# Kernel optimization log

Measured on AMD Instinct MI355X. Metric: run time of the kernel, lower is better.

The kernel has to match this reference:

```python
import jax, jax.numpy as jnp
import numpy as np

ALPHA = 0.5
INV_COEFF = 25.0
STD_COEFF = 25.0
COV_COEFF = 1.0
NUM_MATCHES = 50
EPS = 1e-5
GAMMA = 1.0


def _cdist(a, b):
    # (B,M,C),(B,N,C) -> (B,M,N) euclidean, matmul-based like torch.cdist
    a2 = jnp.sum(a * a, axis=-1, keepdims=True)            # (B,M,1)
    b2 = jnp.sum(b * b, axis=-1, keepdims=True)            # (B,N,1)
    d2 = a2 + jnp.swapaxes(b2, -1, -2) - 2.0 * jnp.einsum('bmc,bnc->bmn', a, b)
    return jnp.sqrt(jnp.maximum(d2, 0.0))


def _nn_match(input_maps, candidate_maps, distances, num_matches):
    # topk(k=1, largest=False) == min/argmin over last dim
    nn_dists = jnp.min(distances, axis=-1)                 # (B,M)
    nn_indices = jnp.argmin(distances, axis=-1)            # (B,M)
    # k smallest nn_dists, ascending order
    _, best_input_idx = jax.lax.top_k(-nn_dists, num_matches)   # (B,k)
    best_cand_idx = jnp.take_along_axis(nn_indices, best_input_idx, axis=1)
    filt_in = jnp.take_along_axis(input_maps, best_input_idx[:, :, None], axis=1)
    filt_cand = jnp.take_along_axis(candidate_maps, best_cand_idx[:, :, None], axis=1)
    return filt_in, filt_cand


def _off_diag_sq_sum(c):
    return jnp.sum(c * c) - jnp.sum(jnp.diag(c) ** 2)


def _std_term(x_flat):
    # unbiased variance over sample dim (torch var default)
    std = jnp.sqrt(jnp.var(x_flat, axis=0, ddof=1) + EPS)
    return jnp.mean(jax.nn.relu(GAMMA - std)) / 2.0


def _cov_term(x_flat):
    n, c = x_flat.shape
    xc = x_flat - jnp.mean(x_flat, axis=0)
    cov = xc.T @ xc / (n - 1)
    return _off_diag_sq_sum(cov) / c


def _vicreg_global(x, y):
    inv = jnp.mean((x - y) ** 2)
    std = _std_term(x) + _std_term(y)
    cov = _cov_term(x) + _cov_term(y)
    return INV_COEFF * inv + STD_COEFF * std + COV_COEFF * cov


def _vicregl_maps(x, y):
    # x, y: (B, k, C)
    inv = jnp.mean((x - y) ** 2)
    xf = x.reshape(-1, x.shape[-1])
    yf = y.reshape(-1, y.shape[-1])
    std = _std_term(xf) + _std_term(yf)
    cov = _cov_term(xf) + _cov_term(yf)
    return INV_COEFF * inv, STD_COEFF * std, COV_COEFF * cov


def _local_loss(spatial_1, spatial_2):
    B, C, H, W = spatial_1.shape
    maps_1 = spatial_1.reshape(B, C, H * W).transpose(0, 2, 1)   # (B,HW,C)
    maps_2 = spatial_2.reshape(B, C, H * W).transpose(0, 2, 1)
    d12 = _cdist(maps_1, maps_2)
    m1f, m1n = _nn_match(maps_1, maps_2, d12, NUM_MATCHES)
    d21 = _cdist(maps_2, maps_1)
    m2f, m2n = _nn_match(maps_2, maps_1, d21, NUM_MATCHES)
    inv1, var1, cov1 = _vicregl_maps(m1f, m1n)
    inv2, var2, cov2 = _vicregl_maps(m2f, m2n)
    return (inv1 + inv2) / 2 + (var1 + var2) / 2 + (cov1 + cov2) / 2


def setup_inputs() -> dict:
    key = jax.random.key(0)
    k1, k2, k3, k4 = jax.random.split(key, 4)
    B, C, H, W = 64, 768, 24, 24
    return {
        'spatial_1': jax.random.normal(k1, (B, C, H, W), dtype=jnp.float32),
        'pooled_1': jax.random.normal(k2, (B, C), dtype=jnp.float32),
        'spatial_2': jax.random.normal(k3, (B, C, H, W), dtype=jnp.float32),
        'pooled_2': jax.random.normal(k4, (B, C), dtype=jnp.float32),
    }


def reference(spatial_1, pooled_1, spatial_2, pooled_2):
    global_loss = _vicreg_global(pooled_1, pooled_2)
    local_loss = _local_loss(spatial_1, spatial_2)
    return ALPHA * global_loss + (1.0 - ALPHA) * local_loss
```

## Files before the change

kernel.cpp:

```cpp
#include <hip/hip_runtime.h>
#include <stdint.h>

typedef unsigned long long ull;
typedef unsigned int uint;
typedef unsigned short ushort;

typedef __attribute__((ext_vector_type(8))) short short8;
typedef __attribute__((ext_vector_type(4))) float floatx4;

#define B   64
#define C   768
#define HW  576
#define K   50
#define NLOC (B*K)

#define OFF_SLOTS   0
#define OFF_COLSUM  256
#define OFF_NN1     18688
#define OFF_NN2     313600
#define OFF_SELP    608512
#define OFF_SELQ    634112
#define OFF_NORM    659712
#define OFF_XT      954624
#define OFF_MP      OFF_XT
#define OFF_XGT     114200832
#define OFF_M       133861632

#define SLOT_INVG 0
#define SLOT_STD  1
#define SLOT_COV  7
#define SLOT_INV1 13
#define SLOT_INV2 14

__device__ __forceinline__ ull umin64(ull a, ull b) { return a < b ? a : b; }

__device__ __forceinline__ float bf2f_lo(uint u) { return __uint_as_float(u << 16); }
__device__ __forceinline__ float bf2f_hi(uint u) { return __uint_as_float(u & 0xffff0000u); }
__device__ __forceinline__ float bf2f(ushort u) { return __uint_as_float(((uint)u) << 16); }

__device__ __forceinline__ ushort f2bf(float f) {
    uint u = __float_as_uint(f);
    uint r = (u + 0x7fffu + ((u >> 16) & 1u)) >> 16;
    return (ushort)r;
}

__device__ __forceinline__ float blk_reduce_sum(float v, float* s4) {
    for (int off = 32; off > 0; off >>= 1) v += __shfl_down(v, off, 64);
    int lane = threadIdx.x & 63, w = threadIdx.x >> 6;
    if (lane == 0) s4[w] = v;
    __syncthreads();
    float r = 0.f;
    if (threadIdx.x == 0) r = s4[0] + s4[1] + s4[2] + s4[3];
    return r;
}

__global__ __launch_bounds__(256) void convert_kernel(const float* __restrict__ x1,
                                                      const float* __restrict__ x2,
                                                      ushort* __restrict__ xT,
                                                      float* __restrict__ norm) {
    int z = blockIdx.z;
    int which = z >> 6, b = z & 63;
    const float* X = which ? x2 : x1;
    int p0 = blockIdx.x * 64, c0 = blockIdx.y * 64;
    __shared__ float tile[64][65];
    const float* src = X + ((size_t)b * C + c0) * HW + p0;
    int col = threadIdx.x & 63, r0 = threadIdx.x >> 6;
    for (int rr = r0; rr < 64; rr += 4)
        tile[rr][col] = src[(size_t)rr * HW + col];
    __syncthreads();
    ushort* dst = xT + (((size_t)which * B + b) * HW + p0) * C + c0;
    int cc = (threadIdx.x & 31) * 2, pr0 = threadIdx.x >> 5;
    for (int pr = pr0; pr < 64; pr += 8) {
        ushort2 o;
        o.x = f2bf(tile[cc][pr]);
        o.y = f2bf(tile[cc + 1][pr]);
        *(ushort2*)&dst[(size_t)pr * C + cc] = o;
    }
    int p = threadIdx.x >> 2, g = threadIdx.x & 3;
    float s = 0.f;
    for (int c = g * 16; c < g * 16 + 16; ++c) {
        float v = bf2f(f2bf(tile[c][p]));
        s = fmaf(v, v, s);
    }
    s += __shfl_down(s, 2, 4);
    s += __shfl_down(s, 1, 4);
    if (g == 0) atomicAdd(&norm[((size_t)which * B + b) * HW + p0 + p], s);
}

__global__ __launch_bounds__(256) void cdist_mfma(const ushort* __restrict__ xT,
                                                  const float* __restrict__ norm,
                                                  ull* __restrict__ nn1,
                                                  ull* __restrict__ nn2) {
    int id = blockIdx.x;
    int xcd = id & 7, slot = id >> 3;
    int b = xcd + 8 * (slot / 25);
    int t = slot % 25;
    int qt = t % 5, pt = t / 5;

    const ushort* X1 = xT + (size_t)b * HW * C;
    const ushort* X2 = xT + (size_t)(B + b) * HW * C;

    __shared__ ull pool[4224];
    char* As = (char*)pool;
    char* Bs = As + 16384;

    int tid = threadIdx.x;
    int w = tid >> 6, l = tid & 63;
    int quad = l >> 4, col = l & 15;
    int lrow = l >> 2, pos = l & 3;

    const ushort* gA[2][2]; const ushort* gB[2][2];
    char* dA[2][2]; char* dB[2][2];
#pragma unroll
    for (int n = 0; n < 2; ++n) {
        int sm = w * 32 + n * 16 + lrow;
        int cdat = pos ^ ((sm >> 1) & 3);
        int p = pt * 128 + sm; if (p >= HW) p = HW - 1;
        int q = qt * 128 + sm; if (q >= HW) q = HW - 1;
#pragma unroll
        for (int s = 0; s < 2; ++s) {
            gA[s][n] = X1 + (size_t)p * C + s * 32 + cdat * 8;
            gB[s][n] = X2 + (size_t)q * C + s * 32 + cdat * 8;
            dA[s][n] = As + s * 8192 + w * 2048 + n * 1024;
            dB[s][n] = Bs + s * 8192 + w * 2048 + n * 1024;
        }
    }

    int offA[4], offB[4];
#pragma unroll
    for (int i = 0; i < 4; ++i) {
        int m_loc = (w >> 1) * 64 + i * 16 + col;
        offA[i] = m_loc * 64 + ((quad ^ ((m_loc >> 1) & 3)) * 16);
        int n_loc = (w & 1) * 64 + i * 16 + col;
        offB[i] = n_loc * 64 + ((quad ^ ((n_loc >> 1) & 3)) * 16);
    }

    floatx4 zero = {0.f, 0.f, 0.f, 0.f};
    floatx4 acc[4][4];
#pragma unroll
    for (int i = 0; i < 4; ++i)
#pragma unroll
        for (int j = 0; j < 4; ++j) acc[i][j] = zero;

    for (int k0 = 0; k0 < C; k0 += 64) {
        __syncthreads();
#pragma unroll
        for (int s = 0; s < 2; ++s)
#pragma unroll
            for (int n = 0; n < 2; ++n) {
                __builtin_amdgcn_global_load_lds(
                    (const __attribute__((address_space(1))) void*)(gA[s][n] + k0),
                    (__attribute__((address_space(3))) void*)dA[s][n], 16, 0, 0);
                __builtin_amdgcn_global_load_lds(
                    (const __attribute__((address_space(1))) void*)(gB[s][n] + k0),
                    (__attribute__((address_space(3))) void*)dB[s][n], 16, 0, 0);
            }
        __syncthreads();
#pragma unroll
        for (int s = 0; s < 2; ++s) {
            short8 a[4], bb[4];
#pragma unroll
            for (int i = 0; i < 4; ++i) a[i] = *(const short8*)(As + s * 8192 + offA[i]);
#pragma unroll
            for (int j = 0; j < 4; ++j) bb[j] = *(const short8*)(Bs + s * 8192 + offB[j]);
#pragma unroll
            for (int i = 0; i < 4; ++i)
#pragma unroll
                for (int j = 0; j < 4; ++j)
                    acc[i][j] = __builtin_amdgcn_mfma_f32_16x16x32_bf16(a[i], bb[j], acc[i][j], 0, 0, 0);
        }
    }

    const float* n1g = norm + (size_t)b * HW;
    const float* n2g = norm + (size_t)(B + b) * HW;
    float n1v[4][4]; bool vp[4][4];
    float n2v[4];    bool vq[4];
#pragma unroll
    for (int i = 0; i < 4; ++i)
#pragma unroll
        for (int r = 0; r < 4; ++r) {
            int p = pt * 128 + (w >> 1) * 64 + i * 16 + quad * 4 + r;
            vp[i][r] = (p < HW);
            n1v[i][r] = n1g[p < HW ? p : (HW - 1)];
        }
#pragma unroll
    for (int j = 0; j < 4; ++j) {
        int q = qt * 128 + (w & 1) * 64 + j * 16 + col;
        vq[j] = (q < HW);
        n2v[j] = n2g[q < HW ? q : (HW - 1)];
    }

    __syncthreads();
    typedef ull row33[33];
    row33* red = (row33*)pool;

#pragma unroll
    for (int i = 0; i < 4; ++i)
#pragma unroll
        for (int r = 0; r < 4; ++r) {
            int p_loc = (w >> 1) * 64 + i * 16 + quad * 4 + r;
            ull best = ~0ull;
#pragma unroll
            for (int j = 0; j < 4; ++j) {
                if (!vq[j]) continue;
                float d2 = fmaxf(n1v[i][r] + n2v[j] - 2.0f * acc[i][j][r], 0.0f);
                unsigned q_glob = qt * 128 + (w & 1) * 64 + j * 16 + col;
                best = umin64(best, ((ull)__float_as_uint(d2) << 32) | q_glob);
            }
            red[p_loc][(w & 1) * 16 + col] = best;
        }
    __syncthreads();
    if (tid < 128) {
        int p_glob = pt * 128 + tid;
        ull m = ~0ull;
#pragma unroll
        for (int x = 0; x < 32; ++x) m = umin64(m, red[tid][x]);
        if (p_glob < HW) atomicMin(&nn1[(size_t)b * HW + p_glob], m);
    }
    __syncthreads();
#pragma unroll
    for (int j = 0; j < 4; ++j) {
        int q_loc = (w & 1) * 64 + j * 16 + col;
        ull best = ~0ull;
#pragma unroll
        for (int i = 0; i < 4; ++i)
#pragma unroll
            for (int r = 0; r < 4; ++r) {
                if (!vp[i][r]) continue;
                float d2 = fmaxf(n1v[i][r] + n2v[j] - 2.0f * acc[i][j][r], 0.0f);
                unsigned p_glob = pt * 128 + (w >> 1) * 64 + i * 16 + quad * 4 + r;
                best = umin64(best, ((ull)__float_as_uint(d2) << 32) | p_glob);
            }
        red[q_loc][(w >> 1) * 4 + quad] = best;
    }
    __syncthreads();
    if (tid < 128) {
        int q_glob = qt * 128 + tid;
        ull m = ~0ull;
#pragma unroll
        for (int x = 0; x < 8; ++x) m = umin64(m, red[tid][x]);
        if (q_glob < HW) atomicMin(&nn2[(size_t)b * HW + q_glob], m);
    }
}

__global__ __launch_bounds__(64) void select_topk_wave(const ull* __restrict__ nn1,
                                                       const ull* __restrict__ nn2,
                                                       int* __restrict__ sel_p,
                                                       int* __restrict__ sel_q) {
    int b = blockIdx.x, dir = blockIdx.y;
    const ull* nn = dir ? nn2 : nn1;
    int lane = threadIdx.x;
    ull key[9]; uint qv[9];
#pragma unroll
    for (int r = 0; r < 9; ++r) {
        int p = r * 64 + lane;
        ull e = nn[(size_t)b * HW + p];
        key[r] = (e & 0xFFFFFFFF00000000ull) | (unsigned)p;
        qv[r] = (uint)(e & 0xFFFFFFFFu);
    }
    int* sp = sel_p + (dir * B + b) * K;
    int* sq = sel_q + (dir * B + b) * K;
    for (int it = 0; it < K; ++it) {
        ull m = key[0];
#pragma unroll
        for (int r = 1; r < 9; ++r) m = umin64(m, key[r]);
#pragma unroll
        for (int off = 32; off > 0; off >>= 1) m = umin64(m, __shfl_xor(m, off, 64));
#pragma unroll
        for (int r = 0; r < 9; ++r) {
            if (key[r] == m) {
                sp[it] = (int)(uint)(m & 0xFFFFFFFFu);
                sq[it] = (int)qv[r];
                key[r] = ~0ull;
            }
        }
    }
}

__global__ __launch_bounds__(256) void gather_jmajor(const ushort* __restrict__ xT,
                                                     const int* __restrict__ sel_p,
                                                     const int* __restrict__ sel_q,
                                                     ushort* __restrict__ XgT) {
    int j = blockIdx.x, s = blockIdx.y;
    int dir = s >> 1;
    int whichsrc = (s == 1 || s == 2) ? 1 : 0;
    const int* sel = (s & 1) ? sel_q : sel_p;
    __shared__ int sidx[64];
    __shared__ uint buf[64][33];
    int tid = threadIdx.x;
    if (tid < 64) sidx[tid] = sel[(dir * B + tid) * K + j];
    __syncthreads();
    int rb = tid >> 2, u = tid & 3;
    const ushort* srow = xT + (((size_t)whichsrc * B + rb) * HW + sidx[rb]) * C;
    int wv = tid >> 6, lb = tid & 63;
    ushort* obase = XgT + (size_t)s * C * NLOC + (size_t)j * 64 + lb;
    for (int ch = 0; ch < 12; ++ch) {
        __syncthreads();
        uint4 v0 = *(const uint4*)(srow + ch * 64 + u * 8);
        uint4 v1 = *(const uint4*)(srow + ch * 64 + (u + 4) * 8);
        buf[rb][u * 4 + 0] = v0.x; buf[rb][u * 4 + 1] = v0.y;
        buf[rb][u * 4 + 2] = v0.z; buf[rb][u * 4 + 3] = v0.w;
        buf[rb][(u + 4) * 4 + 0] = v1.x; buf[rb][(u + 4) * 4 + 1] = v1.y;
        buf[rb][(u + 4) * 4 + 2] = v1.z; buf[rb][(u + 4) * 4 + 3] = v1.w;
        __syncthreads();
#pragma unroll
        for (int st = 0; st < 16; ++st) {
            int cl = wv + st * 4;
            uint uv = buf[lb][cl >> 1];
            ushort val = (cl & 1) ? (ushort)(uv >> 16) : (ushort)(uv & 0xffffu);
            obase[(size_t)(ch * 64 + cl) * NLOC] = val;
        }
    }
}

__global__ __launch_bounds__(256) void ata_mfma(const ushort* __restrict__ XgT,
                                                float* __restrict__ Mp) {
    int bx = blockIdx.x;
    int mat = blockIdx.y, split = blockIdx.z;
    int rt = bx / 6, ct = bx % 6;
    const ushort* X = XgT + (size_t)mat * C * NLOC;

    __shared__ ull pool[4096];
    char* As = (char*)pool;
    char* Bs = As + 16384;

    int tid = threadIdx.x;
    int w = tid >> 6, l = tid & 63;
    int quad = l >> 4, col = l & 15;
    int lrow = l >> 2, pos = l & 3;

    const ushort* gA[2][2]; const ushort* gB[2][2];
    char* dA[2][2]; char* dB[2][2];
#pragma unroll
    for (int n = 0; n < 2; ++n) {
        int sm = w * 32 + n * 16 + lrow;
        int cdat = pos ^ ((sm >> 1) & 3);
#pragma unroll
        for (int s = 0; s < 2; ++s) {
            gA[s][n] = X + (size_t)(rt * 128 + sm) * NLOC + split * 640 + s * 32 + cdat * 8;
            gB[s][n] = X + (size_t)(ct * 128 + sm) * NLOC + split * 640 + s * 32 + cdat * 8;
            dA[s][n] = As + s * 8192 + w * 2048 + n * 1024;
            dB[s][n] = Bs + s * 8192 + w * 2048 + n * 1024;
        }
    }

    int offA[4], offB[4];
#pragma unroll
    for (int i = 0; i < 4; ++i) {
        int m_loc = (w >> 1) * 64 + i * 16 + col;
        offA[i] = m_loc * 64 + ((quad ^ ((m_loc >> 1) & 3)) * 16);
        int n_loc = (w & 1) * 64 + i * 16 + col;
        offB[i] = n_loc * 64 + ((quad ^ ((n_loc >> 1) & 3)) * 16);
    }

    floatx4 zero = {0.f, 0.f, 0.f, 0.f};
    floatx4 acc[4][4];
#pragma unroll
    for (int i = 0; i < 4; ++i)
#pragma unroll
        for (int j = 0; j < 4; ++j) acc[i][j] = zero;

    for (int k0 = 0; k0 < 640; k0 += 64) {
        __syncthreads();
#pragma unroll
        for (int s = 0; s < 2; ++s)
#pragma unroll
            for (int n = 0; n < 2; ++n) {
                __builtin_amdgcn_global_load_lds(
                    (const __attribute__((address_space(1))) void*)(gA[s][n] + k0),
                    (__attribute__((address_space(3))) void*)dA[s][n], 16, 0, 0);
                __builtin_amdgcn_global_load_lds(
                    (const __attribute__((address_space(1))) void*)(gB[s][n] + k0),
                    (__attribute__((address_space(3))) void*)dB[s][n], 16, 0, 0);
            }
        __syncthreads();
#pragma unroll
        for (int s = 0; s < 2; ++s) {
            short8 a[4], bb[4];
#pragma unroll
            for (int i = 0; i < 4; ++i) a[i] = *(const short8*)(As + s * 8192 + offA[i]);
#pragma unroll
            for (int j = 0; j < 4; ++j) bb[j] = *(const short8*)(Bs + s * 8192 + offB[j]);
#pragma unroll
            for (int i = 0; i < 4; ++i)
#pragma unroll
                for (int j = 0; j < 4; ++j)
                    acc[i][j] = __builtin_amdgcn_mfma_f32_16x16x32_bf16(a[i], bb[j], acc[i][j], 0, 0, 0);
        }
    }

    float* Mo = Mp + (size_t)(mat * 5 + split) * C * C;
#pragma unroll
    for (int i = 0; i < 4; ++i)
#pragma unroll
        for (int j = 0; j < 4; ++j)
#pragma unroll
            for (int r = 0; r < 4; ++r) {
                int row = rt * 128 + (w >> 1) * 64 + i * 16 + quad * 4 + r;
                int cc  = ct * 128 + (w & 1) * 64 + j * 16 + col;
                Mo[(size_t)row * C + cc] = acc[i][j][r];
            }
}

__global__ __launch_bounds__(256) void reduce_mp(const float* __restrict__ Mp,
                                                 float* __restrict__ M) {
    int mat = blockIdx.y;
    int i = blockIdx.x * 256 + threadIdx.x;
    float4 r = {0.f, 0.f, 0.f, 0.f};
#pragma unroll
    for (int s = 0; s < 5; ++s) {
        const float4* a = (const float4*)(Mp + (size_t)(mat * 5 + s) * C * C);
        float4 v = a[i];
        r.x += v.x; r.y += v.y; r.z += v.z; r.w += v.w;
    }
    ((float4*)(M + (size_t)mat * C * C))[i] = r;
}

__global__ __launch_bounds__(256) void ata_pooled(const float* __restrict__ p1,
                                                  const float* __restrict__ p2,
                                                  float* __restrict__ M) {
    int mat = 4 + blockIdx.z;
    const float* X = (mat == 4) ? p1 : p2;
    int n = B;
    float* Mo = M + (size_t)mat * C * C;
    int ct = blockIdx.x, rt = blockIdx.y;

    __shared__ float As[16][64];
    __shared__ float Bs[16][64];
    int tid = threadIdx.x;
    int tx = tid & 15, ty = tid >> 4;
    int lr = tid >> 4, lc = (tid & 15) * 4;

    float acc[4][4] = {};
    for (int k0 = 0; k0 < n; k0 += 16) {
        float4 av = *(const float4*)&X[(size_t)(k0 + lr) * C + rt * 64 + lc];
        float4 bv = *(const float4*)&X[(size_t)(k0 + lr) * C + ct * 64 + lc];
        __syncthreads();
        *(float4*)&As[lr][lc] = av;
        *(float4*)&Bs[lr][lc] = bv;
        __syncthreads();
#pragma unroll
        for (int kk = 0; kk < 16; ++kk) {
            float4 af = *(const float4*)&As[kk][ty * 4];
            float4 bf = *(const float4*)&Bs[kk][tx * 4];
            float a[4] = {af.x, af.y, af.z, af.w};
            float bb[4] = {bf.x, bf.y, bf.z, bf.w};
#pragma unroll
            for (int i = 0; i < 4; ++i)
#pragma unroll
                for (int j = 0; j < 4; ++j)
                    acc[i][j] = fmaf(a[i], bb[j], acc[i][j]);
        }
    }
#pragma unroll
    for (int i = 0; i < 4; ++i) {
        float4 o = {acc[i][0], acc[i][1], acc[i][2], acc[i][3]};
        *(float4*)&Mo[(size_t)(rt * 64 + ty * 4 + i) * C + ct * 64 + tx * 4] = o;
    }
}

__global__ __launch_bounds__(256) void colsum4_kernel(const ushort* __restrict__ XgT,
                                                      float* __restrict__ colsum) {
    int mat = blockIdx.y, cb = blockIdx.x * 4;
    int r = threadIdx.x >> 6, lane = threadIdx.x & 63;
    const ushort* row = XgT + ((size_t)mat * C + cb + r) * NLOC;
    float s = 0.f;
    for (int i = lane; i < NLOC; i += 64) s += bf2f(row[i]);
    for (int off = 32; off > 0; off >>= 1) s += __shfl_down(s, off, 64);
    if (lane == 0) colsum[mat * C + cb + r] = s;
}

__global__ __launch_bounds__(256) void colsum_pooled(const float* __restrict__ p1,
                                                     const float* __restrict__ p2,
                                                     float* __restrict__ colsum) {
    int mat = 4 + blockIdx.y;
    const float* X = (mat == 4) ? p1 : p2;
    int c = blockIdx.x * 256 + threadIdx.x;
    float s = 0.f;
    for (int r = 0; r < B; ++r) s += X[(size_t)r * C + c];
    colsum[mat * C + c] = s;
}

__global__ __launch_bounds__(256) void std_kernel(const float* __restrict__ M,
                                                  const float* __restrict__ colsum,
                                                  float* __restrict__ slots) {
    int mat = blockIdx.y;
    float n = (mat < 4) ? (float)NLOC : (float)B;
    int c = blockIdx.x * 256 + threadIdx.x;
    float r = 0.f;
    if (c < C) {
        float mcc = M[(size_t)mat * C * C + (size_t)c * C + c];
        float cs = colsum[mat * C + c];
        float var = (mcc - cs * cs / n) / (n - 1.0f);
        float sd = sqrtf(var + 1e-5f);
        float g = 1.0f - sd;
        r = g > 0.f ? g : 0.f;
    }
    __shared__ float s4[4];
    float t = blk_reduce_sum(r, s4);
    if (threadIdx.x == 0) atomicAdd(&slots[SLOT_STD + mat], t);
}

__global__ __launch_bounds__(256) void cov_kernel(const float* __restrict__ M,
                                                  const float* __restrict__ colsum,
                                                  float* __restrict__ slots) {
    int mat = blockIdx.y;
    float n = (mat < 4) ? (float)NLOC : (float)B;
    float invn1 = 1.0f / (n - 1.0f);
    const float* Mm = M + (size_t)mat * C * C;
    __shared__ float cs_s[C];
    for (int c = threadIdx.x; c < C; c += 256) cs_s[c] = colsum[mat * C + c];
    __syncthreads();
    float s = 0.f;
    int r0 = blockIdx.x * 16;
    for (int r = 0; r < 16; ++r) {
        int row = r0 + r;
        float csr = cs_s[row] / n;
        const float* Mr = Mm + (size_t)row * C;
        for (int c = threadIdx.x; c < C; c += 256) {
            float cv = (Mr[c] - csr * cs_s[c]) * invn1;
            if (c != row) s = fmaf(cv, cv, s);
        }
    }
    __shared__ float s4[4];
    float t = blk_reduce_sum(s, s4);
    if (threadIdx.x == 0) atomicAdd(&slots[SLOT_COV + mat], t);
}

__global__ __launch_bounds__(256) void inv_global_kernel(const float* __restrict__ p1,
                                                         const float* __restrict__ p2,
                                                         float* __restrict__ slots) {
    int idx = blockIdx.x * 256 + threadIdx.x;
    int stride = gridDim.x * 256;
    float s = 0.f;
    for (int i = idx; i < B * C; i += stride) {
        float d = p1[i] - p2[i];
        s = fmaf(d, d, s);
    }
    __shared__ float s4[4];
    float t = blk_reduce_sum(s, s4);
    if (threadIdx.x == 0) atomicAdd(&slots[SLOT_INVG], t);
}

__global__ __launch_bounds__(256) void inv_local2(const ushort* __restrict__ XgT,
                                                  float* __restrict__ slots) {
    int pair = blockIdx.y;
    const uint* A4 = (const uint*)(XgT + (size_t)(2 * pair) * C * NLOC);
    const uint* B4 = (const uint*)(XgT + (size_t)(2 * pair + 1) * C * NLOC);
    int idx = blockIdx.x * 256 + threadIdx.x;
    int stride = gridDim.x * 256;
    int n = C * NLOC / 2;
    float s = 0.f;
    for (int i = idx; i < n; i += stride) {
        uint ua = A4[i], ub = B4[i];
        float d0 = bf2f_lo(ua) - bf2f_lo(ub);
        float d1 = bf2f_hi(ua) - bf2f_hi(ub);
        s = fmaf(d0, d0, s);
        s = fmaf(d1, d1, s);
    }
    __shared__ float s4[4];
    float t = blk_reduce_sum(s, s4);
    if (threadIdx.x == 0) atomicAdd(&slots[(pair == 0) ? SLOT_INV1 : SLOT_INV2], t);
}

__global__ void final_kernel(const float* __restrict__ slots, float* __restrict__ out) {
    float std_t[6], cov_t[6];
    for (int m = 0; m < 6; ++m) {
        std_t[m] = slots[SLOT_STD + m] / (float)C * 0.5f;
        cov_t[m] = slots[SLOT_COV + m] / (float)C;
    }
    float inv_g = slots[SLOT_INVG] / (float)(B * C);
    float global_loss = 25.0f * inv_g + 25.0f * (std_t[4] + std_t[5]) + (cov_t[4] + cov_t[5]);
    float inv1 = 25.0f * slots[SLOT_INV1] / (float)(NLOC * C);
    float inv2 = 25.0f * slots[SLOT_INV2] / (float)(NLOC * C);
    float var1 = 25.0f * (std_t[0] + std_t[1]);
    float var2 = 25.0f * (std_t[2] + std_t[3]);
    float cov1 = cov_t[0] + cov_t[1];
    float cov2 = cov_t[2] + cov_t[3];
    float local_loss = (inv1 + inv2) * 0.5f + (var1 + var2) * 0.5f + (cov1 + cov2) * 0.5f;
    out[0] = 0.5f * global_loss + 0.5f * local_loss;
}

extern "C" void kernel_launch(void* const* d_in, const int* in_sizes, int n_in,
                              void* d_out, int out_size, void* d_ws, size_t ws_size,
                              hipStream_t stream) {
    const float* spatial_1 = (const float*)d_in[0];
    const float* pooled_1  = (const float*)d_in[1];
    const float* spatial_2 = (const float*)d_in[2];
    const float* pooled_2  = (const float*)d_in[3];
    float* out = (float*)d_out;

    char* ws = (char*)d_ws;
    float*  slots  = (float*)(ws + OFF_SLOTS);
    float*  colsum = (float*)(ws + OFF_COLSUM);
    ull*    nn1    = (ull*)(ws + OFF_NN1);
    ull*    nn2    = (ull*)(ws + OFF_NN2);
    int*    sel_p  = (int*)(ws + OFF_SELP);
    int*    sel_q  = (int*)(ws + OFF_SELQ);
    float*  norm   = (float*)(ws + OFF_NORM);
    ushort* xT     = (ushort*)(ws + OFF_XT);
    float*  Mp     = (float*)(ws + OFF_MP);
    ushort* XgT    = (ushort*)(ws + OFF_XGT);
    float*  M      = (float*)(ws + OFF_M);

    hipMemsetAsync(ws, 0, OFF_NN1, stream);
    hipMemsetAsync(ws + OFF_NN1, 0xFF, OFF_SELP - OFF_NN1, stream);
    hipMemsetAsync(ws + OFF_NORM, 0, 294912, stream);

    convert_kernel<<<dim3(9, 12, 128), 256, 0, stream>>>(spatial_1, spatial_2, xT, norm);
    cdist_mfma<<<1600, 256, 0, stream>>>(xT, norm, nn1, nn2);
    select_topk_wave<<<dim3(B, 2), 64, 0, stream>>>(nn1, nn2, sel_p, sel_q);
    gather_jmajor<<<dim3(K, 4), 256, 0, stream>>>(xT, sel_p, sel_q, XgT);
    ata_mfma<<<dim3(36, 4, 5), 256, 0, stream>>>(XgT, Mp);
    ata_pooled<<<dim3(12, 12, 2), 256, 0, stream>>>(pooled_1, pooled_2, M);
    reduce_mp<<<dim3(576, 4), 256, 0, stream>>>(Mp, M);
    colsum4_kernel<<<dim3(192, 4), 256, 0, stream>>>(XgT, colsum);
    colsum_pooled<<<dim3(3, 2), 256, 0, stream>>>(pooled_1, pooled_2, colsum);
    std_kernel<<<dim3(3, 6), 256, 0, stream>>>(M, colsum, slots);
    cov_kernel<<<dim3(48, 6), 256, 0, stream>>>(M, colsum, slots);
    inv_global_kernel<<<dim3(96), 256, 0, stream>>>(pooled_1, pooled_2, slots);
    inv_local2<<<dim3(300, 2), 256, 0, stream>>>(XgT, slots);
    final_kernel<<<1, 1, 0, stream>>>(slots, out);
}
```

Measured before the change: 483.2 us.

## Software-pipeline MFMA GEMM stage loads and rewrite convert kernel register-tiled

The two bf16 MFMA GEMM kernels now share a helper that prefetches the next K-chunk of each LDS stage while computing the other stage, using explicit vmcnt waits and barriers instead of loading both stages and then computing. The convert kernel now has each block handle all channels for 64 positions, transposing 4x4 fragments in registers with a double-buffered load/store sequence. Because of this it writes the squared norms directly, so the atomics and the norm memset go away. The risks are the hand-written waitcnt/barrier ordering and a lower block count in the convert kernel.

Result: no change. 479.9 us (-0.7%).

```diff
diff --git a/kernel.cpp b/kernel.cpp
--- a/kernel.cpp
+++ b/kernel.cpp
@@ -58,33 +58,111 @@
                                                       const float* __restrict__ x2,
                                                       ushort* __restrict__ xT,
                                                       float* __restrict__ norm) {
-    int z = blockIdx.z;
+    int z = blockIdx.y;
     int which = z >> 6, b = z & 63;
-    const float* X = which ? x2 : x1;
-    int p0 = blockIdx.x * 64, c0 = blockIdx.y * 64;
-    __shared__ float tile[64][65];
-    const float* src = X + ((size_t)b * C + c0) * HW + p0;
-    int col = threadIdx.x & 63, r0 = threadIdx.x >> 6;
-    for (int rr = r0; rr < 64; rr += 4)
-        tile[rr][col] = src[(size_t)rr * HW + col];
-    __syncthreads();
-    ushort* dst = xT + (((size_t)which * B + b) * HW + p0) * C + c0;
-    int cc = (threadIdx.x & 31) * 2, pr0 = threadIdx.x >> 5;
-    for (int pr = pr0; pr < 64; pr += 8) {
-        ushort2 o;
-        o.x = f2bf(tile[cc][pr]);
-        o.y = f2bf(tile[cc + 1][pr]);
-        *(ushort2*)&dst[(size_t)pr * C + cc] = o;
-    }
-    int p = threadIdx.x >> 2, g = threadIdx.x & 3;
-    float s = 0.f;
-    for (int c = g * 16; c < g * 16 + 16; ++c) {
-        float v = bf2f(f2bf(tile[c][p]));
-        s = fmaf(v, v, s);
-    }
-    s += __shfl_down(s, 2, 4);
-    s += __shfl_down(s, 1, 4);
-    if (g == 0) atomicAdd(&norm[((size_t)which * B + b) * HW + p0 + p], s);
+    const float* X = (which ? x2 : x1) + (size_t)b * C * HW;
+    int p0 = blockIdx.x * 64;
+    int t = threadIdx.x;
+    int cq = t & 15;
+    int pq = t >> 4;
+    const float* src = X + p0 + 4 * pq;
+    ushort* dstb = xT + (((size_t)which * B + b) * HW + p0) * C;
+    float ss[4] = {0.f, 0.f, 0.f, 0.f};
+
+    floatx4 A[4], Bf[4];
+#define LOADCH(dst, ch)                                                               \
+    {                                                                                 \
+        _Pragma("unroll") for (int i = 0; i < 4; ++i)                                 \
+            dst[i] = *(const floatx4*)(src + (size_t)((ch) * 64 + 4 * cq + i) * HW);  \
+    }
+#define STORECH(sv, ch)                                                               \
+    {                                                                                 \
+        _Pragma("unroll") for (int j = 0; j < 4; ++j) {                               \
+            ushort u0 = f2bf(sv[0][j]), u1 = f2bf(sv[1][j]);                          \
+            ushort u2 = f2bf(sv[2][j]), u3 = f2bf(sv[3][j]);                          \
+            uint2 wv;                                                                 \
+            wv.x = (uint)u0 | ((uint)u1 << 16);                                       \
+            wv.y = (uint)u2 | ((uint)u3 << 16);                                       \
+            *(uint2*)(dstb + (size_t)(4 * pq + j) * C + (ch) * 64 + 4 * cq) = wv;     \
+            float r0 = bf2f(u0), r1 = bf2f(u1), r2 = bf2f(u2), r3 = bf2f(u3);         \
+            ss[j] = fmaf(r0, r0, ss[j]); ss[j] = fmaf(r1, r1, ss[j]);                 \
+            ss[j] = fmaf(r2, r2, ss[j]); ss[j] = fmaf(r3, r3, ss[j]);                 \
+        }                                                                             \
+    }
+
+    LOADCH(A, 0);
+    for (int ch = 0; ch < 12; ch += 2) {
+        LOADCH(Bf, ch + 1);
+        STORECH(A, ch);
+        if (ch + 2 < 12) LOADCH(A, ch + 2);
+        STORECH(Bf, ch + 1);
+    }
+#undef LOADCH
+#undef STORECH
+#pragma unroll
+    for (int j = 0; j < 4; ++j) {
+        ss[j] += __shfl_xor(ss[j], 8, 16);
+        ss[j] += __shfl_xor(ss[j], 4, 16);
+        ss[j] += __shfl_xor(ss[j], 2, 16);
+        ss[j] += __shfl_xor(ss[j], 1, 16);
+    }
+    float outv = (cq == 1) ? ss[1] : (cq == 2) ? ss[2] : (cq == 3) ? ss[3] : ss[0];
+    if (cq < 4)
+        norm[((size_t)which * B + b) * HW + p0 + 4 * pq + cq] = outv;
+}
+
+template<int NK>
+__device__ __forceinline__ void gemm_pp(const ushort* (&gA)[2][2], const ushort* (&gB)[2][2],
+                                        char* (&dA)[2][2], char* (&dB)[2][2],
+                                        const char* As, const char* Bs,
+                                        const int (&offA)[4], const int (&offB)[4],
+                                        floatx4 (&acc)[4][4]) {
+    auto issue = [&](int s, int k0) {
+#pragma unroll
+        for (int n = 0; n < 2; ++n) {
+            __builtin_amdgcn_global_load_lds(
+                (const __attribute__((address_space(1))) void*)(gA[s][n] + k0),
+                (__attribute__((address_space(3))) void*)dA[s][n], 16, 0, 0);
+            __builtin_amdgcn_global_load_lds(
+                (const __attribute__((address_space(1))) void*)(gB[s][n] + k0),
+                (__attribute__((address_space(3))) void*)dB[s][n], 16, 0, 0);
+        }
+    };
+    auto compute = [&](int s) {
+        short8 a[4], bb[4];
+#pragma unroll
+        for (int i = 0; i < 4; ++i) a[i] = *(const short8*)(As + s * 8192 + offA[i]);
+#pragma unroll
+        for (int j = 0; j < 4; ++j) bb[j] = *(const short8*)(Bs + s * 8192 + offB[j]);
+#pragma unroll
+        for (int i = 0; i < 4; ++i)
+#pragma unroll
+            for (int j = 0; j < 4; ++j)
+                acc[i][j] = __builtin_amdgcn_mfma_f32_16x16x32_bf16(a[i], bb[j], acc[i][j], 0, 0, 0);
+    };
+
+    issue(0, 0);
+    issue(1, 0);
+    for (int k = 0; k < NK; ++k) {
+        asm volatile("s_waitcnt vmcnt(4)" ::: "memory");
+        __builtin_amdgcn_s_barrier();
+        __builtin_amdgcn_sched_barrier(0);
+        compute(0);
+        __builtin_amdgcn_sched_barrier(0);
+        __builtin_amdgcn_s_barrier();
+        if (k + 1 < NK) {
+            issue(0, (k + 1) * 64);
+            asm volatile("s_waitcnt vmcnt(4)" ::: "memory");
+        } else {
+            asm volatile("s_waitcnt vmcnt(0)" ::: "memory");
+        }
+        __builtin_amdgcn_s_barrier();
+        __builtin_amdgcn_sched_barrier(0);
+        compute(1);
+        __builtin_amdgcn_sched_barrier(0);
+        __builtin_amdgcn_s_barrier();
+        if (k + 1 < NK) issue(1, (k + 1) * 64);
+    }
 }
 
 __global__ __launch_bounds__(256) void cdist_mfma(const ushort* __restrict__ xT,
@@ -142,34 +220,7 @@
 #pragma unroll
         for (int j = 0; j < 4; ++j) acc[i][j] = zero;
 
-    for (int k0 = 0; k0 < C; k0 += 64) {
-        __syncthreads();
-#pragma unroll
-        for (int s = 0; s < 2; ++s)
-#pragma unroll
-            for (int n = 0; n < 2; ++n) {
-                __builtin_amdgcn_global_load_lds(
-                    (const __attribute__((address_space(1))) void*)(gA[s][n] + k0),
-                    (__attribute__((address_space(3))) void*)dA[s][n], 16, 0, 0);
-                __builtin_amdgcn_global_load_lds(
-                    (const __attribute__((address_space(1))) void*)(gB[s][n] + k0),
-                    (__attribute__((address_space(3))) void*)dB[s][n], 16, 0, 0);
-            }
-        __syncthreads();
-#pragma unroll
-        for (int s = 0; s < 2; ++s) {
-            short8 a[4], bb[4];
-#pragma unroll
-            for (int i = 0; i < 4; ++i) a[i] = *(const short8*)(As + s * 8192 + offA[i]);
-#pragma unroll
-            for (int j = 0; j < 4; ++j) bb[j] = *(const short8*)(Bs + s * 8192 + offB[j]);
-#pragma unroll
-            for (int i = 0; i < 4; ++i)
-#pragma unroll
-                for (int j = 0; j < 4; ++j)
-                    acc[i][j] = __builtin_amdgcn_mfma_f32_16x16x32_bf16(a[i], bb[j], acc[i][j], 0, 0, 0);
-        }
-    }
+    gemm_pp<12>(gA, gB, dA, dB, As, Bs, offA, offB, acc);
 
     const float* n1g = norm + (size_t)b * HW;
     const float* n2g = norm + (size_t)(B + b) * HW;
@@ -360,34 +411,7 @@
 #pragma unroll
         for (int j = 0; j < 4; ++j) acc[i][j] = zero;
 
-    for (int k0 = 0; k0 < 640; k0 += 64) {
-        __syncthreads();
-#pragma unroll
-        for (int s = 0; s < 2; ++s)
-#pragma unroll
-            for (int n = 0; n < 2; ++n) {
-                __builtin_amdgcn_global_load_lds(
-                    (const __attribute__((address_space(1))) void*)(gA[s][n] + k0),
-                    (__attribute__((address_space(3))) void*)dA[s][n], 16, 0, 0);
-                __builtin_amdgcn_global_load_lds(
-                    (const __attribute__((address_space(1))) void*)(gB[s][n] + k0),
-                    (__attribute__((address_space(3))) void*)dB[s][n], 16, 0, 0);
-            }
-        __syncthreads();
-#pragma unroll
-        for (int s = 0; s < 2; ++s) {
-            short8 a[4], bb[4];
-#pragma unroll
-            for (int i = 0; i < 4; ++i) a[i] = *(const short8*)(As + s * 8192 + offA[i]);
-#pragma unroll
-            for (int j = 0; j < 4; ++j) bb[j] = *(const short8*)(Bs + s * 8192 + offB[j]);
-#pragma unroll
-            for (int i = 0; i < 4; ++i)
-#pragma unroll
-                for (int j = 0; j < 4; ++j)
-                    acc[i][j] = __builtin_amdgcn_mfma_f32_16x16x32_bf16(a[i], bb[j], acc[i][j], 0, 0, 0);
-        }
-    }
+    gemm_pp<10>(gA, gB, dA, dB, As, Bs, offA, offB, acc);
 
     float* Mo = Mp + (size_t)(mat * 5 + split) * C * C;
 #pragma unroll
@@ -605,9 +629,8 @@
 
     hipMemsetAsync(ws, 0, OFF_NN1, stream);
     hipMemsetAsync(ws + OFF_NN1, 0xFF, OFF_SELP - OFF_NN1, stream);
-    hipMemsetAsync(ws + OFF_NORM, 0, 294912, stream);
-
-    convert_kernel<<<dim3(9, 12, 128), 256, 0, stream>>>(spatial_1, spatial_2, xT, norm);
+
+    convert_kernel<<<dim3(9, 128), 256, 0, stream>>>(spatial_1, spatial_2, xT, norm);
     cdist_mfma<<<1600, 256, 0, stream>>>(xT, norm, nn1, nn2);
     select_topk_wave<<<dim3(B, 2), 64, 0, stream>>>(nn1, nn2, sel_p, sel_q);
     gather_jmajor<<<dim3(K, 4), 256, 0, stream>>>(xT, sel_p, sel_q, XgT);
```
